# Optimization experiments

Measured on AMD Instinct MI355X. Metric: run time of the kernel, lower is better.

Reference implementation:

```python
import jax, jax.numpy as jnp
import numpy as np

MARGIN = 0.3
EPS = 1e-6      # torch F.pairwise_distance eps used inside TripletMarginLoss
BIG = 1000000.0  # same sentinel as original code


def setup_inputs() -> dict:
    key = jax.random.key(0)
    k1, k2 = jax.random.split(key)
    embeddings = jax.random.normal(k1, (4096, 2048), dtype=jnp.float32)
    labels = jax.random.randint(k2, (4096,), 0, 128)  # 128 identities -> ~32 samples each
    return {"embeddings": embeddings, "labels": labels}


def _batch_hard_triplet_loss(emb, labels):
    B = emb.shape[0]
    # pairwise euclidean distances (torch.cdist p=2)
    sq = jnp.sum(emb * emb, axis=1)                      # [B]
    d2 = sq[:, None] + sq[None, :] - 2.0 * (emb @ emb.T)  # [B,B]
    dists = jnp.sqrt(jnp.maximum(d2, 0.0))

    same = labels[:, None] == labels[None, :]            # [B,B] bool
    eye = jnp.eye(B, dtype=bool)
    pos_mask = same & ~eye

    # hard positive: argmax over same-label (self set to -1, others-with-diff-label masked to 0*d -> use -1 uniformly for non-positives, matching dists*mask_pos with diag=-1 since dists>=0)
    pos_d = jnp.where(pos_mask, dists, -1.0)
    hard_pos = jnp.argmax(pos_d, axis=1)                 # [B]
    # hard negative: argmin over different-label (same-label gets +1e6 like original)
    neg_d = jnp.where(same, dists + BIG, dists)
    hard_neg = jnp.argmin(neg_d, axis=1)                 # [B]

    # valid anchors: at least one positive (other than self) and one negative
    valid = (jnp.sum(pos_mask, axis=1) > 0) & (jnp.sum(~same, axis=1) > 0)

    # TripletMarginLoss recomputes distances with eps added to the difference
    dp = jnp.linalg.norm(emb - emb[hard_pos] + EPS, axis=1)
    dn = jnp.linalg.norm(emb - emb[hard_neg] + EPS, axis=1)
    per = jnp.maximum(dp - dn + MARGIN, 0.0)

    cnt = jnp.sum(valid)
    total = jnp.sum(jnp.where(valid, per, 0.0))
    return jnp.where(cnt > 0, total / jnp.maximum(cnt, 1).astype(per.dtype), 0.0)


def reference(embeddings, labels):
    return _batch_hard_triplet_loss(embeddings, labels)
```

## Files before the change

kernel.cpp:

```cpp
#include <hip/hip_runtime.h>
#include <stdint.h>

#define B 4096
#define D 2048
#define BK 128
#define NITER (D / BK)

typedef unsigned long long ull;
typedef float f32x4 __attribute__((ext_vector_type(4)));

#define SENT_P 0x00000000FFFFFFFFull
#define SENT_N (~0ull)

__device__ __forceinline__ void async_copy16(const unsigned char* g, unsigned char* l) {
  __builtin_amdgcn_global_load_lds(
      (const __attribute__((address_space(1))) unsigned int*)g,
      (__attribute__((address_space(3))) unsigned int*)l,
      16, 0, 0);
}

__global__ void k_convert_sq(const float* __restrict__ emb,
                             unsigned char* __restrict__ embq,
                             float* __restrict__ sq,
                             float* __restrict__ rs,
                             ull* __restrict__ bp,
                             ull* __restrict__ bn) {
  const int row = blockIdx.x, t = threadIdx.x;
  const float4* src = (const float4*)(emb + (size_t)row * D);
  float4 v0 = src[2 * t], v1 = src[2 * t + 1];
  float s = v0.x * v0.x + v0.y * v0.y + v0.z * v0.z + v0.w * v0.w
          + v1.x * v1.x + v1.y * v1.y + v1.z * v1.z + v1.w * v1.w;
  float sm = v0.x + v0.y + v0.z + v0.w + v1.x + v1.y + v1.z + v1.w;

  unsigned w0 = __builtin_amdgcn_cvt_pk_fp8_f32(v0.x, v0.y, 0, false);
  w0 = __builtin_amdgcn_cvt_pk_fp8_f32(v0.z, v0.w, w0, true);
  unsigned w1 = __builtin_amdgcn_cvt_pk_fp8_f32(v1.x, v1.y, 0, false);
  w1 = __builtin_amdgcn_cvt_pk_fp8_f32(v1.z, v1.w, w1, true);
  uint2 o; o.x = w0; o.y = w1;
  ((uint2*)(embq + (size_t)row * D))[t] = o;

  for (int off = 32; off; off >>= 1) {
    s  += __shfl_down(s, off, 64);
    sm += __shfl_down(sm, off, 64);
  }
  __shared__ float ps[4], pm[4];
  int lane = t & 63, wave = t >> 6;
  if (lane == 0) { ps[wave] = s; pm[wave] = sm; }
  __syncthreads();
  if (t == 0) {
    sq[row] = ps[0] + ps[1] + ps[2] + ps[3];
    rs[row] = pm[0] + pm[1] + pm[2] + pm[3];
    bp[row] = SENT_P;
    bn[row] = SENT_N;
  }
}

__launch_bounds__(256, 4)
__global__ void k_gemm_select(const unsigned char* __restrict__ embq,
                              const float* __restrict__ sq,
                              const int* __restrict__ labels,
                              ull* __restrict__ best_pos,
                              ull* __restrict__ best_neg) {
  __shared__ unsigned char ldsA[64 * BK];
  __shared__ unsigned char ldsB[128 * BK];

  int rem = blockIdx.x, p = 0;
  while (rem >= 2 * (32 - p)) { rem -= 2 * (32 - p); ++p; }
  int by = 2 * p;
  int c = 32 - p;
  if (rem >= c) { by += 1; rem -= c; }
  const int bx = p + rem;

  const int tid  = threadIdx.x;
  const int lane = tid & 63;
  const int wave = tid >> 6;
  const int wm = wave >> 1, wn = wave & 1;
  const int q = lane >> 4, m15 = lane & 15;
  const int ibase = by * 64, jbase = bx * 128;

  int aoff[4][2], boff[4][4];
#pragma unroll
  for (int s = 0; s < 4; ++s) {
#pragma unroll
    for (int xg = 0; xg < 2; ++xg) {
      int row = wm * 32 + xg * 16 + m15;
      aoff[s][xg] = row * BK + (((s * 2 + (q >> 1)) ^ (row & 7)) * 16) + (q & 1) * 8;
    }
#pragma unroll
    for (int xg = 0; xg < 4; ++xg) {
      int row = wn * 64 + xg * 16 + m15;
      boff[s][xg] = row * BK + (((s * 2 + (q >> 1)) ^ (row & 7)) * 16) + (q & 1) * 8;
    }
  }

  const int srow = lane >> 3;
  const int slot = lane & 7;

  f32x4 acc[2][4];
  const f32x4 z = {0.f, 0.f, 0.f, 0.f};
#pragma unroll
  for (int a = 0; a < 2; ++a)
#pragma unroll
    for (int b = 0; b < 4; ++b) acc[a][b] = z;

  for (int kb = 0; kb < D; kb += BK) {
    __syncthreads();
#pragma unroll
    for (int pp = 0; pp < 2; ++pp) {
      int r0  = wave * 16 + pp * 8;
      int row = r0 + srow;
      int g   = (slot ^ (row & 7)) * 16;
      const unsigned char* ga = embq + (size_t)(ibase + row) * D + kb + g;
      async_copy16(ga, &ldsA[r0 * BK]);
    }
#pragma unroll
    for (int pp = 0; pp < 4; ++pp) {
      int r0  = wave * 32 + pp * 8;
      int row = r0 + srow;
      int g   = (slot ^ (row & 7)) * 16;
      const unsigned char* gb = embq + (size_t)(jbase + row) * D + kb + g;
      async_copy16(gb, &ldsB[r0 * BK]);
    }
    __syncthreads();

#pragma unroll
    for (int s = 0; s < 4; ++s) {
      long af[2];
      long bfr[4];
#pragma unroll
      for (int xg = 0; xg < 2; ++xg) af[xg] = *(const long*)&ldsA[aoff[s][xg]];
#pragma unroll
      for (int xg = 0; xg < 4; ++xg) bfr[xg] = *(const long*)&ldsB[boff[s][xg]];
#pragma unroll
      for (int mi = 0; mi < 2; ++mi)
#pragma unroll
        for (int ni = 0; ni < 4; ++ni)
          acc[mi][ni] = __builtin_amdgcn_mfma_f32_16x16x32_fp8_fp8(
              af[mi], bfr[ni], acc[mi][ni], 0, 0, 0);
    }
  }

  float sqj[4];
  int labj[4];
#pragma unroll
  for (int ni = 0; ni < 4; ++ni) {
    int jj = jbase + wn * 64 + ni * 16 + m15;
    sqj[ni] = sq[jj];
    labj[ni] = labels[jj];
  }

  ull colBp[4], colBn[4];
#pragma unroll
  for (int ni = 0; ni < 4; ++ni) { colBp[ni] = SENT_P; colBn[ni] = SENT_N; }

#pragma unroll
  for (int mi = 0; mi < 2; ++mi) {
#pragma unroll
    for (int r = 0; r < 4; ++r) {
      const int i = ibase + wm * 32 + mi * 16 + q * 4 + r;
      const float si = sq[i];
      const int li = labels[i];
      ull bp = SENT_P;
      ull bn = SENT_N;
#pragma unroll
      for (int ni = 0; ni < 4; ++ni) {
        int jj = jbase + wn * 64 + ni * 16 + m15;
        if (jj > i) {
          float dot = acc[mi][ni][r];
          float d2 = si + sqj[ni] - 2.0f * dot;
          float dist = sqrtf(fmaxf(d2, 0.0f));
          ull pv = ((ull)__float_as_uint(dist)) << 32;
          if (labj[ni] == li) {
            ull cr = pv | (unsigned)(~jj);
            bp = bp > cr ? bp : cr;
            ull cc = pv | (unsigned)(~i);
            colBp[ni] = colBp[ni] > cc ? colBp[ni] : cc;
          } else {
            ull cr = pv | (unsigned)jj;
            bn = bn < cr ? bn : cr;
            ull cc = pv | (unsigned)i;
            colBn[ni] = colBn[ni] < cc ? colBn[ni] : cc;
          }
        }
      }
#pragma unroll
      for (int off = 1; off <= 8; off <<= 1) {
        ull op = __shfl_xor(bp, off, 64);
        ull on = __shfl_xor(bn, off, 64);
        bp = bp > op ? bp : op;
        bn = bn < on ? bn : on;
      }
      if (m15 == 0) {
        if (bp != SENT_P) atomicMax(&best_pos[i], bp);
        if (bn != SENT_N) atomicMin(&best_neg[i], bn);
      }
    }
  }

#pragma unroll
  for (int ni = 0; ni < 4; ++ni) {
    ull cp = colBp[ni], cn = colBn[ni];
#pragma unroll
    for (int off = 16; off <= 32; off <<= 1) {
      ull op = __shfl_xor(cp, off, 64);
      ull on = __shfl_xor(cn, off, 64);
      cp = cp > op ? cp : op;
      cn = cn < on ? cn : on;
    }
    if (q == 0) {
      int j = jbase + wn * 64 + ni * 16 + m15;
      if (cp != SENT_P) atomicMax(&best_pos[j], cp);
      if (cn != SENT_N) atomicMin(&best_neg[j], cn);
    }
  }
}

__global__ void k_loss_final(const ull* __restrict__ best_pos,
                             const ull* __restrict__ best_neg,
                             const float* __restrict__ rs,
                             float* __restrict__ out) {
  float per = 0.0f;
  int v = 0;
  for (int i = threadIdx.x; i < B; i += 1024) {
    ull bp = best_pos[i], bn = best_neg[i];
    if (bp != SENT_P && bn != SENT_N) {
      unsigned pRaw = ~(unsigned)bp;
      unsigned nRaw = (unsigned)bn;
      int pi = pRaw < (unsigned)B ? (int)pRaw : 0;
      int ni = nRaw < (unsigned)B ? (int)nRaw : 0;
      float distp = __uint_as_float((unsigned)(bp >> 32));
      float distn = __uint_as_float((unsigned)(bn >> 32));
      float ri = rs[i];
      const float e = 1e-6f, de2 = (float)D * 1e-12f;
      float dp2 = distp * distp + 2.0f * e * (ri - rs[pi]) + de2;
      float dn2 = distn * distn + 2.0f * e * (ri - rs[ni]) + de2;
      float dp = sqrtf(fmaxf(dp2, 0.0f));
      float dn = sqrtf(fmaxf(dn2, 0.0f));
      per += fmaxf(dp - dn + 0.3f, 0.0f);
      v += 1;
    }
  }
  for (int off = 32; off; off >>= 1) {
    per += __shfl_down(per, off, 64);
    v   += __shfl_down(v, off, 64);
  }
  __shared__ float pps[16];
  __shared__ int pvs[16];
  int lane = threadIdx.x & 63, wave = threadIdx.x >> 6;
  if (lane == 0) { pps[wave] = per; pvs[wave] = v; }
  __syncthreads();
  if (threadIdx.x == 0) {
    float t = 0.f;
    int cv = 0;
#pragma unroll
    for (int w = 0; w < 16; ++w) { t += pps[w]; cv += pvs[w]; }
    out[0] = cv > 0 ? t / (float)cv : 0.0f;
  }
}

extern "C" void kernel_launch(void* const* d_in, const int* in_sizes, int n_in,
                              void* d_out, int out_size, void* d_ws, size_t ws_size,
                              hipStream_t stream) {
  const float* emb = (const float*)d_in[0];
  const int* labels = (const int*)d_in[1];
  float* out = (float*)d_out;
  char* ws = (char*)d_ws;

  const size_t off_embq = 0;
  const size_t off_sq   = off_embq + (size_t)B * D;
  const size_t off_rs   = off_sq + (size_t)B * 4;
  const size_t off_bp   = off_rs + (size_t)B * 4;
  const size_t off_bn   = off_bp + (size_t)B * 8;

  unsigned char* embq = (unsigned char*)(ws + off_embq);
  float* sq   = (float*)(ws + off_sq);
  float* rs   = (float*)(ws + off_rs);
  ull* bp     = (ull*)(ws + off_bp);
  ull* bn     = (ull*)(ws + off_bn);

  hipLaunchKernelGGL(k_convert_sq, dim3(B), dim3(256), 0, stream,
                     emb, embq, sq, rs, bp, bn);
  hipLaunchKernelGGL(k_gemm_select, dim3(1056), dim3(256), 0, stream,
                     embq, sq, labels, bp, bn);
  hipLaunchKernelGGL(k_loss_final, dim3(1), dim3(1024), 0, stream,
                     bp, bn, rs, out);
}
```

Baseline: 127.8 us.

## Enlarge GEMM tile to 128x128 and double-buffer LDS with async prefetch

The FP8 Gram GEMM tile grows from 64x128 to 128x128, and the triangular grid shrinks from 1056 to 528 blocks. Each wave now does 4x4 MFMA tiles, which gives more data reuse per LDS load. Two LDS buffers are loaded asynchronously so the next K-slice arrives while the current one is computed, with explicit vmcnt waits, raw barriers and s_setprio around the MFMA bursts. The cost is more registers and LDS per block, lowering occupancy to 2 blocks, plus fewer blocks to balance across CUs.

```diff
diff --git a/kernel.cpp b/kernel.cpp
--- a/kernel.cpp
+++ b/kernel.cpp
@@ -5,6 +5,8 @@
 #define D 2048
 #define BK 128
 #define NITER (D / BK)
+#define BM 128
+#define BN 128
 
 typedef unsigned long long ull;
 typedef float f32x4 __attribute__((ext_vector_type(4)));
@@ -55,88 +57,120 @@
   }
 }
 
-__launch_bounds__(256, 4)
+__launch_bounds__(256, 2)
 __global__ void k_gemm_select(const unsigned char* __restrict__ embq,
                               const float* __restrict__ sq,
                               const int* __restrict__ labels,
                               ull* __restrict__ best_pos,
                               ull* __restrict__ best_neg) {
-  __shared__ unsigned char ldsA[64 * BK];
-  __shared__ unsigned char ldsB[128 * BK];
-
-  int rem = blockIdx.x, p = 0;
-  while (rem >= 2 * (32 - p)) { rem -= 2 * (32 - p); ++p; }
-  int by = 2 * p;
-  int c = 32 - p;
-  if (rem >= c) { by += 1; rem -= c; }
-  const int bx = p + rem;
+  __shared__ unsigned char ldsA0[BM * BK];
+  __shared__ unsigned char ldsB0[BN * BK];
+  __shared__ unsigned char ldsA1[BM * BK];
+  __shared__ unsigned char ldsB1[BN * BK];
+
+  int rem = blockIdx.x, by = 0;
+  while (rem >= 32 - by) { rem -= 32 - by; ++by; }
+  const int bx = by + rem;
 
   const int tid  = threadIdx.x;
   const int lane = tid & 63;
   const int wave = tid >> 6;
   const int wm = wave >> 1, wn = wave & 1;
   const int q = lane >> 4, m15 = lane & 15;
-  const int ibase = by * 64, jbase = bx * 128;
-
-  int aoff[4][2], boff[4][4];
+  const int ibase = by * BM, jbase = bx * BN;
+
+  int aoff[4][4], boff[4][4];
 #pragma unroll
   for (int s = 0; s < 4; ++s) {
 #pragma unroll
-    for (int xg = 0; xg < 2; ++xg) {
-      int row = wm * 32 + xg * 16 + m15;
-      aoff[s][xg] = row * BK + (((s * 2 + (q >> 1)) ^ (row & 7)) * 16) + (q & 1) * 8;
-    }
-#pragma unroll
-    for (int xg = 0; xg < 4; ++xg) {
-      int row = wn * 64 + xg * 16 + m15;
-      boff[s][xg] = row * BK + (((s * 2 + (q >> 1)) ^ (row & 7)) * 16) + (q & 1) * 8;
+    for (int g = 0; g < 4; ++g) {
+      int ra = wm * 64 + g * 16 + m15;
+      aoff[s][g] = ra * BK + (((s * 2 + (q >> 1)) ^ (ra & 7)) * 16) + (q & 1) * 8;
+      int rb = wn * 64 + g * 16 + m15;
+      boff[s][g] = rb * BK + (((s * 2 + (q >> 1)) ^ (rb & 7)) * 16) + (q & 1) * 8;
     }
   }
 
   const int srow = lane >> 3;
   const int slot = lane & 7;
-
-  f32x4 acc[2][4];
+  size_t agoff[4], bgoff[4];
+  int ldst[4];
+#pragma unroll
+  for (int pp = 0; pp < 4; ++pp) {
+    int r0  = wave * 32 + pp * 8;
+    int row = r0 + srow;
+    int gg  = (slot ^ (row & 7)) * 16;
+    agoff[pp] = (size_t)(ibase + row) * D + gg;
+    bgoff[pp] = (size_t)(jbase + row) * D + gg;
+    ldst[pp]  = r0 * BK;
+  }
+
+  f32x4 acc[4][4];
   const f32x4 z = {0.f, 0.f, 0.f, 0.f};
 #pragma unroll
-  for (int a = 0; a < 2; ++a)
+  for (int a = 0; a < 4; ++a)
 #pragma unroll
     for (int b = 0; b < 4; ++b) acc[a][b] = z;
 
-  for (int kb = 0; kb < D; kb += BK) {
-    __syncthreads();
-#pragma unroll
-    for (int pp = 0; pp < 2; ++pp) {
-      int r0  = wave * 16 + pp * 8;
-      int row = r0 + srow;
-      int g   = (slot ^ (row & 7)) * 16;
-      const unsigned char* ga = embq + (size_t)(ibase + row) * D + kb + g;
-      async_copy16(ga, &ldsA[r0 * BK]);
-    }
-#pragma unroll
-    for (int pp = 0; pp < 4; ++pp) {
-      int r0  = wave * 32 + pp * 8;
-      int row = r0 + srow;
-      int g   = (slot ^ (row & 7)) * 16;
-      const unsigned char* gb = embq + (size_t)(jbase + row) * D + kb + g;
-      async_copy16(gb, &ldsB[r0 * BK]);
-    }
-    __syncthreads();
-
+  auto stage = [&](unsigned char* LA, unsigned char* LB, int kb) {
+#pragma unroll
+    for (int pp = 0; pp < 4; ++pp)
+      async_copy16(embq + agoff[pp] + kb, &LA[ldst[pp]]);
+#pragma unroll
+    for (int pp = 0; pp < 4; ++pp)
+      async_copy16(embq + bgoff[pp] + kb, &LB[ldst[pp]]);
+  };
+
+  auto compute = [&](const unsigned char* LA, const unsigned char* LB) {
 #pragma unroll
     for (int s = 0; s < 4; ++s) {
-      long af[2];
-      long bfr[4];
-#pragma unroll
-      for (int xg = 0; xg < 2; ++xg) af[xg] = *(const long*)&ldsA[aoff[s][xg]];
-#pragma unroll
-      for (int xg = 0; xg < 4; ++xg) bfr[xg] = *(const long*)&ldsB[boff[s][xg]];
-#pragma unroll
-      for (int mi = 0; mi < 2; ++mi)
+      long af[4], bf[4];
+#pragma unroll
+      for (int g = 0; g < 4; ++g) af[g] = *(const long*)&LA[aoff[s][g]];
+#pragma unroll
+      for (int g = 0; g < 4; ++g) bf[g] = *(const long*)&LB[boff[s][g]];
+      __builtin_amdgcn_s_setprio(1);
+#pragma unroll
+      for (int mi = 0; mi < 4; ++mi)
 #pragma unroll
         for (int ni = 0; ni < 4; ++ni)
           acc[mi][ni] = __builtin_amdgcn_mfma_f32_16x16x32_fp8_fp8(
-              af[mi], bfr[ni], acc[mi][ni], 0, 0, 0);
+              af[mi], bf[ni], acc[mi][ni], 0, 0, 0);
+      __builtin_amdgcn_s_setprio(0);
+    }
+  };
+
+  stage(ldsA0, ldsB0, 0);
+  stage(ldsA1, ldsB1, BK);
+  asm volatile("s_waitcnt vmcnt(8)" ::: "memory");
+  __builtin_amdgcn_s_barrier();
+  asm volatile("" ::: "memory");
+
+  for (int t = 0; t < NITER; t += 2) {
+    compute(ldsA0, ldsB0);
+    asm volatile("" ::: "memory");
+    __builtin_amdgcn_s_barrier();
+    if (t + 2 < NITER) {
+      stage(ldsA0, ldsB0, (t + 2) * BK);
+      asm volatile("s_waitcnt vmcnt(8)" ::: "memory");
+    } else {
+      asm volatile("s_waitcnt vmcnt(0)" ::: "memory");
+    }
+    __builtin_amdgcn_s_barrier();
+    asm volatile("" ::: "memory");
+
+    compute(ldsA1, ldsB1);
+    if (t + 2 < NITER) {
+      asm volatile("" ::: "memory");
+      __builtin_amdgcn_s_barrier();
+      if (t + 3 < NITER) {
+        stage(ldsA1, ldsB1, (t + 3) * BK);
+        asm volatile("s_waitcnt vmcnt(8)" ::: "memory");
+      } else {
+        asm volatile("s_waitcnt vmcnt(0)" ::: "memory");
+      }
+      __builtin_amdgcn_s_barrier();
+      asm volatile("" ::: "memory");
     }
   }
 
@@ -154,10 +188,10 @@
   for (int ni = 0; ni < 4; ++ni) { colBp[ni] = SENT_P; colBn[ni] = SENT_N; }
 
 #pragma unroll
-  for (int mi = 0; mi < 2; ++mi) {
+  for (int mi = 0; mi < 4; ++mi) {
 #pragma unroll
     for (int r = 0; r < 4; ++r) {
-      const int i = ibase + wm * 32 + mi * 16 + q * 4 + r;
+      const int i = ibase + wm * 64 + mi * 16 + q * 4 + r;
       const float si = sq[i];
       const int li = labels[i];
       ull bp = SENT_P;
@@ -280,7 +314,7 @@
 
   hipLaunchKernelGGL(k_convert_sq, dim3(B), dim3(256), 0, stream,
                      emb, embq, sq, rs, bp, bn);
-  hipLaunchKernelGGL(k_gemm_select, dim3(1056), dim3(256), 0, stream,
+  hipLaunchKernelGGL(k_gemm_select, dim3(528), dim3(256), 0, stream,
                      embq, sq, labels, bp, bn);
   hipLaunchKernelGGL(k_loss_final, dim3(1), dim3(1024), 0, stream,
                      bp, bn, rs, out);
```

Result: slower. 154.2 us (+20.7%).

## Permute fp8 K layout so each lane loads 16-byte fragments from LDS

Applied to the files above, without the earlier changes.

The conversion kernel now writes fp8 rows in a permuted K order, so each lane's data for two consecutive MFMA k-steps sits in one contiguous 16-byte chunk. The GEMM reads 128-bit vectors from LDS instead of 64-bit ones, which halves the number of LDS read instructions, and it issues MFMAs on the two halves. Global-load address offsets are also hoisted out of the K loop. Because the dot product is invariant under a consistent permutation of K, the results stay the same, provided the write permutation matches the read pattern exactly.

```diff
diff --git a/kernel.cpp b/kernel.cpp
--- a/kernel.cpp
+++ b/kernel.cpp
@@ -5,9 +5,12 @@
 #define D 2048
 #define BK 128
 #define NITER (D / BK)
+#define BM 64
+#define BN 128
 
 typedef unsigned long long ull;
 typedef float f32x4 __attribute__((ext_vector_type(4)));
+typedef long v2l __attribute__((ext_vector_type(2)));
 
 #define SENT_P 0x00000000FFFFFFFFull
 #define SENT_N (~0ull)
@@ -37,7 +40,8 @@
   unsigned w1 = __builtin_amdgcn_cvt_pk_fp8_f32(v1.x, v1.y, 0, false);
   w1 = __builtin_amdgcn_cvt_pk_fp8_f32(v1.z, v1.w, w1, true);
   uint2 o; o.x = w0; o.y = w1;
-  ((uint2*)(embq + (size_t)row * D))[t] = o;
+  const int pos = ((t >> 4) << 7) | ((t & 3) << 5) | (((t >> 2) & 3) << 3);
+  *(uint2*)(embq + (size_t)row * D + pos) = o;
 
   for (int off = 32; off; off >>= 1) {
     s  += __shfl_down(s, off, 64);
@@ -61,8 +65,8 @@
                               const int* __restrict__ labels,
                               ull* __restrict__ best_pos,
                               ull* __restrict__ best_neg) {
-  __shared__ unsigned char ldsA[64 * BK];
-  __shared__ unsigned char ldsB[128 * BK];
+  __shared__ __align__(16) unsigned char ldsA[BM * BK];
+  __shared__ __align__(16) unsigned char ldsB[BN * BK];
 
   int rem = blockIdx.x, p = 0;
   while (rem >= 2 * (32 - p)) { rem -= 2 * (32 - p); ++p; }
@@ -76,25 +80,41 @@
   const int wave = tid >> 6;
   const int wm = wave >> 1, wn = wave & 1;
   const int q = lane >> 4, m15 = lane & 15;
-  const int ibase = by * 64, jbase = bx * 128;
-
-  int aoff[4][2], boff[4][4];
-#pragma unroll
-  for (int s = 0; s < 4; ++s) {
-#pragma unroll
-    for (int xg = 0; xg < 2; ++xg) {
-      int row = wm * 32 + xg * 16 + m15;
-      aoff[s][xg] = row * BK + (((s * 2 + (q >> 1)) ^ (row & 7)) * 16) + (q & 1) * 8;
-    }
-#pragma unroll
-    for (int xg = 0; xg < 4; ++xg) {
-      int row = wn * 64 + xg * 16 + m15;
-      boff[s][xg] = row * BK + (((s * 2 + (q >> 1)) ^ (row & 7)) * 16) + (q & 1) * 8;
+  const int ibase = by * BM, jbase = bx * BN;
+
+  int aoff[2][2], boff[2][4];
+#pragma unroll
+  for (int sh = 0; sh < 2; ++sh) {
+#pragma unroll
+    for (int g = 0; g < 2; ++g) {
+      int ra = wm * 32 + g * 16 + m15;
+      aoff[sh][g] = ra * BK + (((q * 2 + sh) ^ (ra & 7)) * 16);
+    }
+#pragma unroll
+    for (int g = 0; g < 4; ++g) {
+      int rb = wn * 64 + g * 16 + m15;
+      boff[sh][g] = rb * BK + (((q * 2 + sh) ^ (rb & 7)) * 16);
     }
   }
 
   const int srow = lane >> 3;
   const int slot = lane & 7;
+  size_t agoff[2], bgoff[4];
+  int lasta[2], lastb[4];
+#pragma unroll
+  for (int pp = 0; pp < 2; ++pp) {
+    int r0  = wave * 16 + pp * 8;
+    int row = r0 + srow;
+    agoff[pp] = (size_t)(ibase + row) * D + (slot ^ (row & 7)) * 16;
+    lasta[pp] = r0 * BK;
+  }
+#pragma unroll
+  for (int pp = 0; pp < 4; ++pp) {
+    int r0  = wave * 32 + pp * 8;
+    int row = r0 + srow;
+    bgoff[pp] = (size_t)(jbase + row) * D + (slot ^ (row & 7)) * 16;
+    lastb[pp] = r0 * BK;
+  }
 
   f32x4 acc[2][4];
   const f32x4 z = {0.f, 0.f, 0.f, 0.f};
@@ -106,37 +126,32 @@
   for (int kb = 0; kb < D; kb += BK) {
     __syncthreads();
 #pragma unroll
-    for (int pp = 0; pp < 2; ++pp) {
-      int r0  = wave * 16 + pp * 8;
-      int row = r0 + srow;
-      int g   = (slot ^ (row & 7)) * 16;
-      const unsigned char* ga = embq + (size_t)(ibase + row) * D + kb + g;
-      async_copy16(ga, &ldsA[r0 * BK]);
-    }
-#pragma unroll
-    for (int pp = 0; pp < 4; ++pp) {
-      int r0  = wave * 32 + pp * 8;
-      int row = r0 + srow;
-      int g   = (slot ^ (row & 7)) * 16;
-      const unsigned char* gb = embq + (size_t)(jbase + row) * D + kb + g;
-      async_copy16(gb, &ldsB[r0 * BK]);
-    }
+    for (int pp = 0; pp < 2; ++pp)
+      async_copy16(embq + agoff[pp] + kb, &ldsA[lasta[pp]]);
+#pragma unroll
+    for (int pp = 0; pp < 4; ++pp)
+      async_copy16(embq + bgoff[pp] + kb, &ldsB[lastb[pp]]);
     __syncthreads();
 
 #pragma unroll
-    for (int s = 0; s < 4; ++s) {
-      long af[2];
-      long bfr[4];
-#pragma unroll
-      for (int xg = 0; xg < 2; ++xg) af[xg] = *(const long*)&ldsA[aoff[s][xg]];
-#pragma unroll
-      for (int xg = 0; xg < 4; ++xg) bfr[xg] = *(const long*)&ldsB[boff[s][xg]];
+    for (int sh = 0; sh < 2; ++sh) {
+      v2l af[2], bf[4];
+#pragma unroll
+      for (int g = 0; g < 2; ++g) af[g] = *(const v2l*)&ldsA[aoff[sh][g]];
+#pragma unroll
+      for (int g = 0; g < 4; ++g) bf[g] = *(const v2l*)&ldsB[boff[sh][g]];
 #pragma unroll
       for (int mi = 0; mi < 2; ++mi)
 #pragma unroll
         for (int ni = 0; ni < 4; ++ni)
           acc[mi][ni] = __builtin_amdgcn_mfma_f32_16x16x32_fp8_fp8(
-              af[mi], bfr[ni], acc[mi][ni], 0, 0, 0);
+              af[mi][0], bf[ni][0], acc[mi][ni], 0, 0, 0);
+#pragma unroll
+      for (int mi = 0; mi < 2; ++mi)
+#pragma unroll
+        for (int ni = 0; ni < 4; ++ni)
+          acc[mi][ni] = __builtin_amdgcn_mfma_f32_16x16x32_fp8_fp8(
+              af[mi][1], bf[ni][1], acc[mi][ni], 0, 0, 0);
     }
   }
 
```

Result: faster. 122.1 us (median of 2 runs) (-4.5%).
